# Optimization experiments

Hardware: AMD Instinct MI355X
Metric: run time of the kernel (lower is better)

## Reference

```python
import jax, jax.numpy as jnp
import numpy as np

ORDER = 12      # Coef_num in the original
BLOCK = 1024
N_FFT = 2046    # torch.stft(n_fft=2046) -> 1024 onesided bins
HOP = 511       # torch default n_fft // 4
WORN = 1024
G1, G2 = 0.92, 0.6


def burg_lpc(y):
    """Burg's method LPC (exactly librosa.lpc), vectorized over blocks. y: [B, N] -> [B, ORDER+1]."""
    ar = jnp.zeros((y.shape[0], ORDER + 1), y.dtype).at[:, 0].set(1.0)
    f = y[:, 1:]
    b = y[:, :-1]
    den = jnp.sum(f * f, -1) + jnp.sum(b * b, -1)
    for i in range(ORDER):
        k = -2.0 * jnp.sum(b * f, -1) / den                     # reflection coeff [B]
        js = np.arange(1, i + 2)
        ar = ar.at[:, js].set(ar[:, js] + k[:, None] * ar[:, i - js + 1])
        f_new = f + k[:, None] * b
        b = b + k[:, None] * f
        f = f_new
        den = (1.0 - k * k) * den - b[:, -1] ** 2 - f[:, 0] ** 2
        f = f[:, 1:]
        b = b[:, :-1]
    return ar


def perceptual_weights(y):
    """Stacked |freqz| weight matrix [n_blocks*11, 1024], matching the original append order."""
    n_blocks = y.shape[0] // BLOCK
    yb = y[: n_blocks * BLOCK].reshape(n_blocks, BLOCK)
    lpc = burg_lpc(yb)[:, :ORDER]                               # original drops coeff index 12
    j = np.arange(ORDER)
    a1 = (lpc * (G1 ** j)).astype(jnp.complex64)                # denominator coeffs (bandwidth-expanded)
    a2 = (lpc * (G2 ** j)).astype(jnp.complex64)                # numerator coeffs
    omega = jnp.pi * jnp.arange(WORN) / WORN                    # freqz worN=1024 digital freqs
    E = jnp.exp(-1j * omega[:, None] * j[None, :]).astype(jnp.complex64)   # [F, 12]
    # freqz is called inside the k1 loop: at step k1 only coeffs 0..k1 are filled -> triangular mask
    M = jnp.asarray(j[None, :] <= np.arange(1, ORDER)[:, None], jnp.complex64)  # [11, 12]
    num = jnp.einsum('bj,kj,fj->bkf', a2, M, E)
    den = jnp.einsum('bj,kj,fj->bkf', a1, M, E)
    return jnp.abs(num / den).reshape(n_blocks * (ORDER - 1), WORN)


def stft_mag(x):
    """torch.stft(x, n_fft=2046, center=True, reflect pad, rect window, onesided) magnitude -> [1024, n_frames]."""
    pad = N_FFT // 2
    xp = jnp.pad(x, (pad, pad), mode='reflect')
    n_frames = 1 + x.shape[0] // HOP
    idx = jnp.arange(n_frames)[:, None] * HOP + jnp.arange(N_FFT)[None, :]
    frames = xp[idx]                                            # [n_frames, 2046]
    return jnp.abs(jnp.fft.rfft(frames, axis=1)).T              # [1024, n_frames]


def setup_inputs() -> dict:
    key = jax.random.key(0)
    kx, ky = jax.random.split(key)
    L = 2048 * 1024
    x = jax.random.normal(kx, (L,), dtype=jnp.float32)
    y = jax.random.normal(ky, (L,), dtype=jnp.float32)
    return {"x": x, "y": y}


def reference(x, y):
    W = jax.lax.stop_gradient(perceptual_weights(y))            # original computes weights on detached numpy
    Sx = stft_mag(x)
    Sy = stft_mag(y)
    mse = jnp.mean((Sx - Sy) ** 2, axis=1)                      # [1024] per-frequency-bin MSE over frames
    return jnp.mean(mse[None, :] / W)                           # broadcast over [n_blocks*11, 1024]
```

## Files before the change

kernel.cpp:

```cpp
#include <hip/hip_runtime.h>
#include <hip/hip_bf16.h>

#define PI_D 3.14159265358979323846
#define L_TOTAL 2097152
#define NFRAMES 4105
#define NBLK    4108
#define MROWS_P 8216
#define MPAD    8320
#define KP      512
#define NDIM    2048
#define PSTRIDE 8224

#define COMBINE_BLOCKS 4352
#define INVW_BLOCKS 512


#define BURG_BLOCKS   512
#define FRAMES_BLOCKS 2080
#define BASIS_BLOCKS  512
#define SARR_BLOCKS   17
#define PREP_BLOCKS   (BURG_BLOCKS + FRAMES_BLOCKS + BASIS_BLOCKS + SARR_BLOCKS)

typedef __attribute__((ext_vector_type(8))) short short8;
typedef __attribute__((ext_vector_type(4))) short short4v;
typedef __attribute__((ext_vector_type(4))) float floatx4;

typedef __attribute__((address_space(1))) void gvoid_as1;
typedef __attribute__((address_space(3))) void lvoid_as3;

__device__ __forceinline__ void gld_lds16(const void* g, void* l) {
    __builtin_amdgcn_global_load_lds((gvoid_as1*)g, (lvoid_as3*)l, 16, 0, 0);
}

__device__ __forceinline__ float b2f(short v) {
    unsigned int u = ((unsigned int)(unsigned short)v) << 16;
    return __uint_as_float(u);
}

__device__ __forceinline__ float xorall(float v) {
    v += __shfl_xor(v, 1, 64);
    v += __shfl_xor(v, 2, 64);
    v += __shfl_xor(v, 4, 64);
    v += __shfl_xor(v, 8, 64);
    v += __shfl_xor(v, 16, 64);
    v += __shfl_xor(v, 32, 64);
    return v;
}

__device__ __forceinline__ float wave_reduce(float v) {
    v += __shfl_down(v, 32, 64);
    v += __shfl_down(v, 16, 64);
    v += __shfl_down(v, 8, 64);
    v += __shfl_down(v, 4, 64);
    v += __shfl_down(v, 2, 64);
    v += __shfl_down(v, 1, 64);
    return v;
}

__device__ __forceinline__ void frames_body(int bid, int tid,
                                            const float* __restrict__ x,
                                            const float* __restrict__ y,
                                            __hip_bfloat16* __restrict__ A) {
    const int ci = bid * 256 + tid;
    const int rb = ci >> 10;
    const int kc = (ci >> 4) & 63;
    const int rowIn = ci & 15;
    const int row = rb * 16 + rowIn;
    __hip_bfloat16 tmp[8];
    if (row < MROWS_P) {
        const int b = row >> 1;
        const float* src = (row & 1) ? y : x;
        const int base = b * 511 + kc * 8 - 1023;
#pragma unroll
        for (int e = 0; e < 8; e++) {
            const int n = kc * 8 + e;
            float v = 0.f;
            if (n < 511) {
                int p = base + e;
                if (p < 0) p = -p;
                else if (p >= L_TOTAL) p = 2 * L_TOTAL - 2 - p;
                v = src[p];
            }
            tmp[e] = __float2bfloat16(v);
        }
    } else {
#pragma unroll
        for (int e = 0; e < 8; e++) tmp[e] = __float2bfloat16(0.f);
    }
    *(short8*)((char*)A + (size_t)ci * 16) = *(short8*)tmp;
}

__device__ __forceinline__ void basis_body(int bid, int tid,
                                           __hip_bfloat16* __restrict__ Bt) {
    const int ci = bid * 256 + tid;
    const int rb = ci >> 10;
    const int kc = (ci >> 4) & 63;
    const int rowIn = ci & 15;
    const int row = rb * 16 + rowIn;
    const int f = row >> 1;
    const bool isSin = row & 1;
    const int n0 = kc * 8;
    const int m0 = (f * n0) % 2046;
    float s, c, ss, cs;
    __sincosf((float)m0 * (float)(PI_D / 1023.0), &s, &c);
    __sincosf((float)f * (float)(PI_D / 1023.0), &ss, &cs);
    __hip_bfloat16 tmp[8];
#pragma unroll
    for (int e = 0; e < 8; e++) {
        const int n = n0 + e;
        float v = isSin ? -s : c;
        if (n >= 511) v = 0.f;
        tmp[e] = __float2bfloat16(v);
        float c2 = c * cs - s * ss;
        float s2 = s * cs + c * ss;
        c = c2; s = s2;
    }
    *(short8*)((char*)Bt + (size_t)ci * 16) = *(short8*)tmp;
}

__device__ __forceinline__ void sarr_body(int bid, int tid,
                                          const float* __restrict__ x,
                                          const float* __restrict__ y,
                                          float4* __restrict__ S) {
    const int b = bid * 256 + tid;
    int p0 = 511 * b - 1023;
    int p1 = p0 + 1;
    int m0 = (p0 < 0) ? -p0 : ((p0 >= L_TOTAL) ? 2 * L_TOTAL - 2 - p0 : p0);
    int m1 = (p1 < 0) ? -p1 : ((p1 >= L_TOTAL) ? 2 * L_TOTAL - 2 - p1 : p1);
    S[b] = make_float4(x[m0], x[m1], y[m0], y[m1]);
}

__device__ __forceinline__ void burg_body(int bid, int tid,
                                          const float* __restrict__ y,
                                          float* __restrict__ ar_out,
                                          float* __restrict__ wsf) {
    if (bid < 8) wsf[bid * 256 + tid] = 0.f;

    const int lane = tid & 63;
    const int wid = tid >> 6;
    const int blk = bid * 4 + wid;
    const float4* yb4 = (const float4*)(y + (size_t)blk * 1024) + lane * 4;

    float t[16];
#pragma unroll
    for (int q = 0; q < 4; q++) {
        float4 v = yb4[q];
        t[q * 4 + 0] = v.x; t[q * 4 + 1] = v.y;
        t[q * 4 + 2] = v.z; t[q * 4 + 3] = v.w;
    }
    float b[16], f[16];
#pragma unroll
    for (int r = 0; r < 16; r++) b[r] = t[r];
#pragma unroll
    for (int r = 0; r < 15; r++) f[r] = t[r + 1];
    {
        float nb = __shfl_down(t[0], 1, 64);
        f[15] = (lane == 63) ? 0.f : nb;
        if (lane == 63) b[15] = 0.f;
    }

    float den = 0.f;
#pragma unroll
    for (int r = 0; r < 16; r++) den += f[r] * f[r] + b[r] * b[r];
    den = xorall(den);

    float ar_s[13];
    ar_s[0] = 1.f;
#pragma unroll
    for (int j = 1; j < 13; j++) ar_s[j] = 0.f;

#pragma unroll
    for (int i = 0; i < 12; i++) {
        float num = 0.f;
#pragma unroll
        for (int r = 0; r < 16; r++) num += f[r] * b[r];
        num = xorall(num);
        const float k = -2.f * num / den;

        float fu[16], bu[16];
#pragma unroll
        for (int r = 0; r < 16; r++) {
            fu[r] = f[r] + k * b[r];
            bu[r] = b[r] + k * f[r];
        }
        const float f0 = __shfl(fu[0], 0, 64);
        const int pos = 1022 - i;
        const int L = pos >> 4, S = pos & 15;
        const float blast = __shfl(bu[S], L, 64);

        den = (1.f - k * k) * den - blast * blast - f0 * f0;

        float nf = __shfl_down(fu[0], 1, 64);
#pragma unroll
        for (int r = 0; r < 15; r++) f[r] = fu[r + 1];
        f[15] = (lane == 63) ? 0.f : nf;
#pragma unroll
        for (int r = 0; r < 16; r++) b[r] = bu[r];
        if (lane == L) b[S] = 0.f;

        float tmp[13];
#pragma unroll
        for (int js = 1; js <= i + 1; js++) tmp[js] = ar_s[js] + k * ar_s[i + 1 - js];
#pragma unroll
        for (int js = 1; js <= i + 1; js++) ar_s[js] = tmp[js];
    }

#pragma unroll
    for (int j = 0; j < 12; j++)
        if (lane == j) ar_out[(size_t)blk * 12 + j] = ar_s[j];
}

__global__ __launch_bounds__(256) void prep_kernel(const float* __restrict__ x,
                                                   const float* __restrict__ y,
                                                   __hip_bfloat16* __restrict__ A,
                                                   __hip_bfloat16* __restrict__ Bt,
                                                   float4* __restrict__ S,
                                                   float* __restrict__ ar,
                                                   float* __restrict__ wsf) {
    const int bid = blockIdx.x;
    const int tid = threadIdx.x;
    if (bid < BURG_BLOCKS) {
        burg_body(bid, tid, y, ar, wsf);
    } else if (bid < BURG_BLOCKS + FRAMES_BLOCKS) {
        frames_body(bid - BURG_BLOCKS, tid, x, y, A);
    } else if (bid < BURG_BLOCKS + FRAMES_BLOCKS + BASIS_BLOCKS) {
        basis_body(bid - BURG_BLOCKS - FRAMES_BLOCKS, tid, Bt);
    } else {
        sarr_body(bid - BURG_BLOCKS - FRAMES_BLOCKS - BASIS_BLOCKS, tid, x, y, S);
    }
}

__global__ __launch_bounds__(256) void gemm_p_kernel(
    const __hip_bfloat16* __restrict__ A, const __hip_bfloat16* __restrict__ Bt,
    __hip_bfloat16* __restrict__ Pt) {
    __shared__ __align__(16) __hip_bfloat16 Al[128 * 32];
    __shared__ __align__(16) __hip_bfloat16 Bl[128 * 32];

    const int tid = threadIdx.x;
    const int lane = tid & 63;
    const int w = tid >> 6;
    const int wm = w >> 1, wn = w & 1;
    const int q = lane >> 4, l15 = lane & 15;
    const int tileN = blockIdx.x * 128;
    const int tileM = blockIdx.y * 128;

    floatx4 acc[4][4];
#pragma unroll
    for (int i = 0; i < 4; i++)
#pragma unroll
        for (int j = 0; j < 4; j++) acc[i][j] = (floatx4){0.f, 0.f, 0.f, 0.f};

    const int rl = tid & 15;
    const int qq = (tid >> 4) & 3;
    const int gg0 = tid >> 6;
    const char* pA0 = (const char*)A + ((((size_t)(tileM >> 4) + gg0) << 10) + qq * 16 + rl) * 16;
    const char* pA1 = pA0 + (size_t)4 * 16384;
    const char* pB0 = (const char*)Bt + ((((size_t)(tileN >> 4) + gg0) << 10) + qq * 16 + rl) * 16;
    const char* pB1 = pB0 + (size_t)4 * 16384;
    char* AlB = (char*)Al;
    char* BlB = (char*)Bl;

    for (int it = 0; it < KP / 32; it++) {
        gld_lds16(pA0, AlB + tid * 16);
        gld_lds16(pA1, AlB + (tid + 256) * 16);
        gld_lds16(pB0, BlB + tid * 16);
        gld_lds16(pB1, BlB + (tid + 256) * 16);
        pA0 += 1024; pA1 += 1024; pB0 += 1024; pB1 += 1024;
        __syncthreads();

        short8 af[4], bf[4];
#pragma unroll
        for (int sm = 0; sm < 4; sm++)
            af[sm] = *(const short8*)(AlB + (((wm * 4 + sm) * 64 + lane) * 16));
#pragma unroll
        for (int sn = 0; sn < 4; sn++)
            bf[sn] = *(const short8*)(BlB + (((wn * 4 + sn) * 64 + lane) * 16));
#pragma unroll
        for (int sm = 0; sm < 4; sm++)
#pragma unroll
            for (int sn = 0; sn < 4; sn++)
                acc[sm][sn] = __builtin_amdgcn_mfma_f32_16x16x32_bf16(
                    af[sm], bf[sn], acc[sm][sn], 0, 0, 0);
        __syncthreads();
    }

#pragma unroll
    for (int sm = 0; sm < 4; sm++) {
        const int rowBase = tileM + wm * 64 + sm * 16 + q * 4;
        if (rowBase >= MROWS_P) continue;
#pragma unroll
        for (int sn = 0; sn < 4; sn++) {
            const int colG = tileN + wn * 64 + sn * 16 + l15;
            short4v pk;
#pragma unroll
            for (int r = 0; r < 4; r++) {
                __hip_bfloat16 h = __float2bfloat16(acc[sm][sn][r]);
                pk[r] = *(short*)&h;
            }
            *(short4v*)((char*)Pt + ((size_t)colG * PSTRIDE + rowBase) * 2) = pk;
        }
    }
}

__device__ __forceinline__ void combine_body(int bx, int ty, int tid,
                                             const __hip_bfloat16* __restrict__ Pt,
                                             const float4* __restrict__ S,
                                             float* __restrict__ mse_sum) {
    const int lane = tid & 63;
    const int wid = tid >> 6;
    const int f = bx * 4 + wid;

    float wc[4], ws[4];
    wc[0] = 1.f; ws[0] = 0.f;
#pragma unroll
    for (int h = 1; h < 4; h++) {
        int m = (511 * h * f) % 2046;
        float s, c;
        __sincosf((float)m * (float)(PI_D / 1023.0), &s, &c);
        wc[h] = c; ws[h] = -s;
    }
    float wtc0, wts0, wtc1, wts1;
    {
        int m = (2044 * f) % 2046;
        float s, c;
        __sincosf((float)m * (float)(PI_D / 1023.0), &s, &c);
        wtc0 = c; wts0 = -s;
        m = (2045 * f) % 2046;
        __sincosf((float)m * (float)(PI_D / 1023.0), &s, &c);
        wtc1 = c; wts1 = -s;
    }

    const __hip_bfloat16* rowRe = Pt + (size_t)(2 * f) * PSTRIDE;
    const __hip_bfloat16* rowIm = rowRe + PSTRIDE;

    float acc = 0.f;
    const int tt0 = ty * 256 + 4 * lane;
    if (tt0 < NFRAMES) {
        short8 re0 = *(const short8*)(rowRe + 2 * tt0);
        short8 re1 = *(const short8*)(rowRe + 2 * tt0 + 8);
        short8 im0 = *(const short8*)(rowIm + 2 * tt0);
        short8 im1 = *(const short8*)(rowIm + 2 * tt0 + 8);
        float4 sT[4];
#pragma unroll
        for (int d = 0; d < 4; d++) sT[d] = S[tt0 + 4 + d];
        float vr[16], vi[16];
#pragma unroll
        for (int j = 0; j < 8; j++) {
            vr[j] = b2f(re0[j]); vr[j + 8] = b2f(re1[j]);
            vi[j] = b2f(im0[j]); vi[j + 8] = b2f(im1[j]);
        }
#pragma unroll
        for (int d = 0; d < 4; d++) {
            const int tt = tt0 + d;
            if (tt >= NFRAMES) break;
            float xr = 0.f, xi = 0.f, yr = 0.f, yi = 0.f;
#pragma unroll
            for (int h = 0; h < 4; h++) {
                const int qx = 2 * d + 2 * h;
                xr += wc[h] * vr[qx] - ws[h] * vi[qx];
                xi += wc[h] * vi[qx] + ws[h] * vr[qx];
                const int qy = qx + 1;
                yr += wc[h] * vr[qy] - ws[h] * vi[qy];
                yi += wc[h] * vi[qy] + ws[h] * vr[qy];
            }
            const float4 sd = sT[d];
            xr += wtc0 * sd.x + wtc1 * sd.y;
            xi += wts0 * sd.x + wts1 * sd.y;
            yr += wtc0 * sd.z + wtc1 * sd.w;
            yi += wts0 * sd.z + wts1 * sd.w;
            float dm = sqrtf(xr * xr + xi * xi) - sqrtf(yr * yr + yi * yi);
            acc += dm * dm;
        }
    }
    acc = xorall(acc);
    if (lane == 0) atomicAdd(&mse_sum[f], acc);
}

__device__ __forceinline__ void invw_body(int bid, int tid,
                                          const float* __restrict__ ar,
                                          float* __restrict__ invW) {
    __shared__ float sar[16][12];
    const int f = (bid & 3) * 256 + tid;
    const int b0 = (bid >> 2) * 16;
    if (tid < 16 * 12) ((float*)sar)[tid] = ar[(size_t)b0 * 12 + tid];
    __syncthreads();

    const float omega = (float)(PI_D / 1024.0) * (float)f;
    float sw, cw;
    __sincosf(omega, &sw, &cw);

    float acc = 0.f;
#pragma unroll 4
    for (int bb = 0; bb < 16; bb++) {
        float a0 = sar[bb][0];
        float nr = a0, ni = 0.f, dr = a0, di = 0.f;
        float er = 1.f, ei = 0.f;
        float g1p = 1.f, g2p = 1.f;
#pragma unroll
        for (int j = 1; j < 12; j++) {
            float er2 = er * cw + ei * sw;
            float ei2 = ei * cw - er * sw;
            er = er2; ei = ei2;
            g1p *= 0.92f; g2p *= 0.6f;
            float aj = sar[bb][j];
            float a1 = aj * g1p, a2 = aj * g2p;
            nr += a2 * er; ni += a2 * ei;
            dr += a1 * er; di += a1 * ei;
            float D = dr * dr + di * di;
            float Nn = nr * nr + ni * ni;
            acc += D * __builtin_amdgcn_rsqf(D * Nn);
        }
    }
    atomicAdd(&invW[f], acc);
}

__global__ __launch_bounds__(256) void combine_invw_kernel(
    const __hip_bfloat16* __restrict__ Pt,
    const float4* __restrict__ S,
    float* __restrict__ mse_sum,
    const float* __restrict__ ar,
    float* __restrict__ invW) {
    const int bid = blockIdx.x;
    const int tid = threadIdx.x;
    if (bid < INVW_BLOCKS) {
        invw_body(bid, tid, ar, invW);
    } else {
        const int cb = bid - INVW_BLOCKS;
        combine_body(cb & 255, cb >> 8, tid, Pt, S, mse_sum);
    }
}

__global__ void final_kernel(const float* __restrict__ mse_sum,
                             const float* __restrict__ invW,
                             float* __restrict__ out) {
    __shared__ float red[4];
    const int tid = threadIdx.x;
    float lo = 0.f;
    for (int f = tid; f < 1024; f += 256) lo += mse_sum[f] * invW[f];
    lo = wave_reduce(lo);
    if ((tid & 63) == 0) red[tid >> 6] = lo;
    __syncthreads();
    if (tid == 0) {
        float tot = red[0] + red[1] + red[2] + red[3];
        out[0] = tot * (float)(1.0 / (4105.0 * 22528.0 * 1024.0));
    }
}

extern "C" void kernel_launch(void* const* d_in, const int* in_sizes, int n_in,
                              void* d_out, int out_size, void* d_ws, size_t ws_size,
                              hipStream_t stream) {
    const float* x = (const float*)d_in[0];
    const float* y = (const float*)d_in[1];
    float* out = (float*)d_out;

    float* wsf = (float*)d_ws;
    float* mse_sum = wsf;
    float* invW = wsf + 1024;
    float* ar = wsf + 2080;
    float4* S = (float4*)((char*)d_ws + 131072);
    __hip_bfloat16* Ap = (__hip_bfloat16*)((char*)d_ws + 262144);
    __hip_bfloat16* Bp = (__hip_bfloat16*)((char*)d_ws + 8781824);
    __hip_bfloat16* Pt = (__hip_bfloat16*)((char*)d_ws + 10878976);

    prep_kernel<<<PREP_BLOCKS, 256, 0, stream>>>(x, y, Ap, Bp, S, ar, wsf);
    gemm_p_kernel<<<dim3(NDIM / 128, MPAD / 128), 256, 0, stream>>>(Ap, Bp, Pt);
    combine_invw_kernel<<<INVW_BLOCKS + COMBINE_BLOCKS, 256, 0, stream>>>(Pt, S, mse_sum, ar, invW);
    final_kernel<<<1, 256, 0, stream>>>(mse_sum, invW, out);
}
```

Baseline: 133.4 us.

## Use 8-wave GEMM blocks and vectorize frame extraction loads

The GEMM kernel moves from 4 waves to 8 waves per 128x128 tile. Each wave now owns a 32x64 sub-tile instead of 64x64, which halves accumulator registers per thread and each thread issues one LDS-direct load per operand per K step. The frame-building kernel remaps threads so that consecutive threads take consecutive k-chunks of the same row, and uses two unaligned float4 loads on the interior fast path instead of eight scalar reflect-checked loads. The aim is higher occupancy and latency hiding in the GEMM and coalesced, vectorized reads in the prep stage. The cost is more waves contending for each barrier and more total LDS fragment reads per tile.

```diff
diff --git a/kernel.cpp b/kernel.cpp
--- a/kernel.cpp
+++ b/kernel.cpp
@@ -24,6 +24,7 @@
 typedef __attribute__((ext_vector_type(8))) short short8;
 typedef __attribute__((ext_vector_type(4))) short short4v;
 typedef __attribute__((ext_vector_type(4))) float floatx4;
+typedef float floatx4u __attribute__((ext_vector_type(4), aligned(4)));
 
 typedef __attribute__((address_space(1))) void gvoid_as1;
 typedef __attribute__((address_space(3))) void lvoid_as3;
@@ -61,27 +62,36 @@
                                             const float* __restrict__ x,
                                             const float* __restrict__ y,
                                             __hip_bfloat16* __restrict__ A) {
-    const int ci = bid * 256 + tid;
-    const int rb = ci >> 10;
-    const int kc = (ci >> 4) & 63;
-    const int rowIn = ci & 15;
+    const int rb = bid >> 2;
+    const int kc = (bid & 3) * 16 + (tid & 15);
+    const int rowIn = tid >> 4;
     const int row = rb * 16 + rowIn;
+    const int ci = rb * 1024 + kc * 16 + rowIn;
     __hip_bfloat16 tmp[8];
     if (row < MROWS_P) {
         const int b = row >> 1;
         const float* src = (row & 1) ? y : x;
-        const int base = b * 511 + kc * 8 - 1023;
-#pragma unroll
-        for (int e = 0; e < 8; e++) {
-            const int n = kc * 8 + e;
-            float v = 0.f;
-            if (n < 511) {
-                int p = base + e;
-                if (p < 0) p = -p;
-                else if (p >= L_TOTAL) p = 2 * L_TOTAL - 2 - p;
-                v = src[p];
+        const int p0 = b * 511 + kc * 8 - 1023;
+        if (kc < 63 && p0 >= 0 && p0 + 8 <= L_TOTAL) {
+            floatx4u v0 = *(const floatx4u*)(src + p0);
+            floatx4u v1 = *(const floatx4u*)(src + p0 + 4);
+#pragma unroll
+            for (int e = 0; e < 4; e++) tmp[e] = __float2bfloat16(v0[e]);
+#pragma unroll
+            for (int e = 0; e < 4; e++) tmp[4 + e] = __float2bfloat16(v1[e]);
+        } else {
+#pragma unroll
+            for (int e = 0; e < 8; e++) {
+                const int n = kc * 8 + e;
+                float v = 0.f;
+                if (n < 511) {
+                    int p = p0 + e;
+                    if (p < 0) p = -p;
+                    else if (p >= L_TOTAL) p = 2 * L_TOTAL - 2 - p;
+                    v = src[p];
+                }
+                tmp[e] = __float2bfloat16(v);
             }
-            tmp[e] = __float2bfloat16(v);
         }
     } else {
 #pragma unroll
@@ -230,7 +240,7 @@
     }
 }
 
-__global__ __launch_bounds__(256) void gemm_p_kernel(
+__global__ __launch_bounds__(512, 4) void gemm_p_kernel(
     const __hip_bfloat16* __restrict__ A, const __hip_bfloat16* __restrict__ Bt,
     __hip_bfloat16* __restrict__ Pt) {
     __shared__ __align__(16) __hip_bfloat16 Al[128 * 32];
@@ -239,44 +249,40 @@
     const int tid = threadIdx.x;
     const int lane = tid & 63;
     const int w = tid >> 6;
-    const int wm = w >> 1, wn = w & 1;
+    const int wm = w >> 1;
+    const int wn = w & 1;
     const int q = lane >> 4, l15 = lane & 15;
     const int tileN = blockIdx.x * 128;
     const int tileM = blockIdx.y * 128;
 
-    floatx4 acc[4][4];
-#pragma unroll
-    for (int i = 0; i < 4; i++)
+    floatx4 acc[2][4];
+#pragma unroll
+    for (int i = 0; i < 2; i++)
 #pragma unroll
         for (int j = 0; j < 4; j++) acc[i][j] = (floatx4){0.f, 0.f, 0.f, 0.f};
 
-    const int rl = tid & 15;
-    const int qq = (tid >> 4) & 3;
-    const int gg0 = tid >> 6;
-    const char* pA0 = (const char*)A + ((((size_t)(tileM >> 4) + gg0) << 10) + qq * 16 + rl) * 16;
-    const char* pA1 = pA0 + (size_t)4 * 16384;
-    const char* pB0 = (const char*)Bt + ((((size_t)(tileN >> 4) + gg0) << 10) + qq * 16 + rl) * 16;
-    const char* pB1 = pB0 + (size_t)4 * 16384;
+    const int gg = tid >> 6;
+    const int inner = tid & 63;
+    const char* pA = (const char*)A + ((((size_t)(tileM >> 4) + gg) << 10) + inner) * 16;
+    const char* pB = (const char*)Bt + ((((size_t)(tileN >> 4) + gg) << 10) + inner) * 16;
     char* AlB = (char*)Al;
     char* BlB = (char*)Bl;
 
     for (int it = 0; it < KP / 32; it++) {
-        gld_lds16(pA0, AlB + tid * 16);
-        gld_lds16(pA1, AlB + (tid + 256) * 16);
-        gld_lds16(pB0, BlB + tid * 16);
-        gld_lds16(pB1, BlB + (tid + 256) * 16);
-        pA0 += 1024; pA1 += 1024; pB0 += 1024; pB1 += 1024;
+        gld_lds16(pA, AlB + tid * 16);
+        gld_lds16(pB, BlB + tid * 16);
+        pA += 1024; pB += 1024;
         __syncthreads();
 
-        short8 af[4], bf[4];
-#pragma unroll
-        for (int sm = 0; sm < 4; sm++)
-            af[sm] = *(const short8*)(AlB + (((wm * 4 + sm) * 64 + lane) * 16));
+        short8 af[2], bf[4];
+#pragma unroll
+        for (int sm = 0; sm < 2; sm++)
+            af[sm] = *(const short8*)(AlB + (((wm * 2 + sm) * 64 + lane) * 16));
 #pragma unroll
         for (int sn = 0; sn < 4; sn++)
             bf[sn] = *(const short8*)(BlB + (((wn * 4 + sn) * 64 + lane) * 16));
 #pragma unroll
-        for (int sm = 0; sm < 4; sm++)
+        for (int sm = 0; sm < 2; sm++)
 #pragma unroll
             for (int sn = 0; sn < 4; sn++)
                 acc[sm][sn] = __builtin_amdgcn_mfma_f32_16x16x32_bf16(
@@ -285,8 +291,8 @@
     }
 
 #pragma unroll
-    for (int sm = 0; sm < 4; sm++) {
-        const int rowBase = tileM + wm * 64 + sm * 16 + q * 4;
+    for (int sm = 0; sm < 2; sm++) {
+        const int rowBase = tileM + wm * 32 + sm * 16 + q * 4;
         if (rowBase >= MROWS_P) continue;
 #pragma unroll
         for (int sn = 0; sn < 4; sn++) {
@@ -463,7 +469,7 @@
     __hip_bfloat16* Pt = (__hip_bfloat16*)((char*)d_ws + 10878976);
 
     prep_kernel<<<PREP_BLOCKS, 256, 0, stream>>>(x, y, Ap, Bp, S, ar, wsf);
-    gemm_p_kernel<<<dim3(NDIM / 128, MPAD / 128), 256, 0, stream>>>(Ap, Bp, Pt);
+    gemm_p_kernel<<<dim3(NDIM / 128, MPAD / 128), 512, 0, stream>>>(Ap, Bp, Pt);
     combine_invw_kernel<<<INVW_BLOCKS + COMBINE_BLOCKS, 256, 0, stream>>>(Pt, S, mse_sum, ar, invW);
     final_kernel<<<1, 256, 0, stream>>>(mse_sum, invW, out);
 }
```

After: 128.0 us. 1.04x faster.
